# Kernel optimization log

Hardware: AMD Instinct MI355X
Metric: run time of the kernel (lower is better)

Reference implementation:

```python
import jax, jax.numpy as jnp
import numpy as np

EPS = 1e-5

# The 8 fixed sobel kernels from the original module. Summing convolutions with
# the same input equals one convolution with the summed kernel, so we embed the
# four 3x3 kernels (pad=1) into 5x5 (pad=2) and precombine everything into a
# single depthwise 5x5 kernel (exactly the math of detect_edge_1/2 summed).
_K3 = [
    [[2, 4, 2], [0, 0, 0], [-2, -4, -2]],
    [[4, 2, 0], [2, 0, -2], [0, -2, -4]],
    [[2, 0, -2], [4, 0, -4], [2, 0, -2]],
    [[0, -2, -4], [2, 0, -2], [4, 2, 0]],
]
_K5 = [
    [[0, 0, 0, 0, 0], [0, -2, -4, -2, 0], [-1, -4, 0, 4, 1], [0, 2, 4, 2, 0], [0, 0, 0, 0, 0]],
    [[0, 0, -1, 0, 0], [0, -2, -4, 2, 0], [0, -4, 0, 4, 0], [0, -2, 4, 2, 0], [0, 0, 1, 0, 0]],
    [[0, 0, 1, 0, 0], [0, -2, 4, 2, 0], [0, -4, 0, 4, 0], [0, -2, -4, 2, 0], [0, 0, -1, 0, 0]],
    [[0, 0, 0, 0, 0], [0, 2, 4, 2, 0], [-1, -4, 0, 4, 1], [0, -2, -4, -2, 0], [0, 0, 0, 0, 0]],
]

def _combined_sobel_kernel():
    k = np.zeros((5, 5), dtype=np.float32)
    for k3 in _K3:
        k[1:4, 1:4] += np.asarray(k3, dtype=np.float32)
    for k5 in _K5:
        k += np.asarray(k5, dtype=np.float32)
    return jnp.asarray(k)

SOBEL_K = _combined_sobel_kernel()  # [5,5]


def _conv2d(x, w, b, pad):
    # x: [N,C,H,W], w: [O,I,kh,kw]
    y = jax.lax.conv_general_dilated(
        x, w, window_strides=(1, 1), padding=[(pad, pad), (pad, pad)],
        dimension_numbers=('NCHW', 'OIHW', 'NCHW'))
    return y + b[None, :, None, None]


def _bn_relu(y, gamma, beta):
    # BatchNorm2d in training mode: per-channel batch stats over (N,H,W),
    # biased variance, eps=1e-5.
    m = jnp.mean(y, axis=(0, 2, 3), keepdims=True)
    v = jnp.mean(jnp.square(y - m), axis=(0, 2, 3), keepdims=True)
    yn = (y - m) * jax.lax.rsqrt(v + EPS)
    return jax.nn.relu(yn * gamma[None, :, None, None] + beta[None, :, None, None])


def _single_conv(x, w, b, gamma, beta, pad):
    return _bn_relu(_conv2d(x, w, b, pad), gamma, beta)


def _sobel(x):
    # Fused depthwise conv replacing the per-channel loops over 8 kernels.
    C = x.shape[1]
    w = jnp.broadcast_to(SOBEL_K[None, None], (C, 1, 5, 5))
    return jax.lax.conv_general_dilated(
        x, w, window_strides=(1, 1), padding=[(2, 2), (2, 2)],
        dimension_numbers=('NCHW', 'OIHW', 'NCHW'), feature_group_count=C)


def setup_inputs() -> dict:
    key = jax.random.key(0)
    ks = jax.random.split(key, 16)
    Cin, Cout = 64, 128
    Ch = Cout // 2
    B, H, W = 8, 160, 160
    s = 0.05
    d = {
        'input_f': jax.random.normal(ks[0], (B, Cin, H, W), jnp.float32),
        'w1': jax.random.normal(ks[1], (Cout, Cin, 1, 1), jnp.float32) * s,
        'b1': jnp.zeros((Cout,), jnp.float32),
        'g1': jnp.ones((Cout,), jnp.float32),
        'be1': jnp.zeros((Cout,), jnp.float32),
        'w2': jax.random.normal(ks[2], (Ch, Cout, 3, 3), jnp.float32) * s,
        'b2': jnp.zeros((Ch,), jnp.float32),
        'g2': jnp.ones((Ch,), jnp.float32),
        'be2': jnp.zeros((Ch,), jnp.float32),
        'w3': jax.random.normal(ks[3], (Ch, Ch, 3, 3), jnp.float32) * s,
        'b3': jnp.zeros((Ch,), jnp.float32),
        'g3': jnp.ones((Ch,), jnp.float32),
        'be3': jnp.zeros((Ch,), jnp.float32),
        'w4': jax.random.normal(ks[4], (Ch, Cin, 3, 3), jnp.float32) * s,
        'b4': jnp.zeros((Ch,), jnp.float32),
        'g4': jnp.ones((Ch,), jnp.float32),
        'be4': jnp.zeros((Ch,), jnp.float32),
    }
    return d


def reference(input_f, w1, b1, g1, be1, w2, b2, g2, be2, w3, b3, g3, be3, w4, b4, g4, be4):
    c1 = _single_conv(input_f, w1, b1, g1, be1, pad=0)   # [B,Cout,H,W]
    c2 = _single_conv(c1, w2, b2, g2, be2, pad=1)        # [B,Cout//2,H,W]
    edge = _sobel(c2)                                    # depthwise sobel sum
    c3 = _single_conv(edge, w3, b3, g3, be3, pad=1)
    skip = _single_conv(input_f, w4, b4, g4, be4, pad=1)
    return jnp.concatenate([skip, c3], axis=1)           # [B,Cout,H,W]
```

## Files before the change

### kernel.cpp

```cpp
#include <hip/hip_runtime.h>

typedef unsigned short u16;
typedef unsigned int u32;
typedef __attribute__((ext_vector_type(8))) short bf16x8;
typedef __attribute__((ext_vector_type(4))) float f32x4;

#define WD 160
#define HW 25600
#define NPIXF 204800.0f
#define BNEPS 1e-5f
#define SLOTB 6553600ll
#define BATB  13107200ll

__device__ __forceinline__ float bf2f(u16 u){ return __uint_as_float(((u32)u)<<16); }
__device__ __forceinline__ u16 f2bf(float f){ u32 x=__float_as_uint(f); return (u16)((x + 0x7FFFu + ((x>>16)&1u))>>16); }
__device__ __forceinline__ u32 pack2(float a,float b){ return (u32)f2bf(a) | ((u32)f2bf(b)<<16); }

__device__ __forceinline__ f32x4 MF(bf16x8 a, bf16x8 b, f32x4 c){
  return __builtin_amdgcn_mfma_f32_16x16x32_bf16(a, b, c, 0, 0, 0);
}
__device__ __forceinline__ void gload16(const void* g, void* l){
  __builtin_amdgcn_global_load_lds((const __attribute__((address_space(1))) void*)(g),
                                   (__attribute__((address_space(3))) void*)(l), 16, 0, 0);
}

__global__ __launch_bounds__(256) void k_prepw(
    const float* __restrict__ w1, const float* __restrict__ w2,
    const float* __restrict__ w3, const float* __restrict__ w4,
    u16* __restrict__ wp1, u16* __restrict__ wp2,
    u16* __restrict__ wp3, u16* __restrict__ wp4)
{
  int t = blockIdx.x*256 + threadIdx.x;
  if (t < 8192){
    int i = t&7, oc = (t>>3)&127, kc = (t>>10)&3, icb = t>>12;
    wp1[t] = f2bf(w1[oc*64 + icb*32 + kc*8 + i]);
  }
  int u = t - 8192;
  if (u >= 0 && u < 73728){
    int i = u&7, oc = (u>>3)&63, kc = (u>>9)&3, v = u>>11;
    int icb = (v*57)>>9; int tap = v - icb*9;
    wp2[u] = f2bf(w2[(oc*128 + icb*32 + kc*8 + i)*9 + tap]);
  }
  int u3 = t - (8192+73728);
  if (u3 >= 0 && u3 < 36864){
    int k = u3&31, oc = (u3>>5)&63, v = u3>>11;
    int icb = (v >= 9) ? 1 : 0; int tap = v - icb*9;
    wp3[u3] = f2bf(w3[(oc*64 + icb*32 + k)*9 + tap]);
    wp4[u3] = f2bf(w4[(oc*64 + icb*32 + k)*9 + tap]);
  }
}

__global__ __launch_bounds__(256,4) void k_conv1(
    const float* __restrict__ x, const u16* __restrict__ wp1,
    char* __restrict__ dout, float* __restrict__ stats, int nslot)
{
  __shared__ __align__(16) char Xs[16384];
  const int tid = threadIdx.x, lane = tid&63, w = tid>>6;
  const int l15 = lane&15, kc = lane>>4;
  int flat = blockIdx.x + 200*blockIdx.y;
  flat = (flat&7)*200 + (flat>>3);
  const int b = flat/200, bx = flat - b*200;
  const int px0 = bx*128;
  const float* xb = x + (size_t)b*64*HW;

#pragma unroll
  for (int q=0; q<4; ++q){
    int s = q*256 + tid;
    int px = s & 127, ck = (s>>7)&3, icb = s>>9;
    const float* pb = xb + (size_t)(icb*32 + ck*8)*HW + px0 + px;
    u32 w4[4];
#pragma unroll
    for (int j=0;j<4;++j)
      w4[j] = pack2(pb[(size_t)(2*j)*HW], pb[(size_t)(2*j+1)*HW]);
    *(uint4*)(Xs + icb*8192 + px*64 + ((ck ^ ((px>>1)&3))<<4))
        = make_uint4(w4[0],w4[1],w4[2],w4[3]);
  }
  __syncthreads();

  f32x4 acc[4][4];
  for (int t=0;t<4;++t) for (int o=0;o<4;++o) acc[t][o] = (f32x4){0.f,0.f,0.f,0.f};
  const int och = (w>>1)*64;
  int a1off[4];
  for (int t=0;t<4;++t){
    int px = (w&1)*64 + t*16 + l15;
    a1off[t] = px*64 + ((kc ^ ((px>>1)&3))<<4);
  }
  __builtin_amdgcn_s_setprio(1);
#pragma unroll
  for (int icb=0; icb<2; ++icb){
    bf16x8 a[4], bw[4];
#pragma unroll
    for (int t=0;t<4;++t) a[t] = *(const bf16x8*)(Xs + icb*8192 + a1off[t]);
#pragma unroll
    for (int o=0;o<4;++o)
      bw[o] = *(const bf16x8*)(wp1 + ((size_t)(icb*4 + kc)*128 + och + o*16 + l15)*8);
#pragma unroll
    for (int t=0;t<4;++t)
#pragma unroll
      for (int o=0;o<4;++o)
        acc[t][o] = MF(a[t], bw[o], acc[t][o]);
  }
  __builtin_amdgcn_s_setprio(0);

  u16* c1 = (u16*)(dout + (size_t)b*BATB);
  float sa[4]={0,0,0,0}, sq[4]={0,0,0,0};
  for (int t=0;t<4;++t){
    int pxb = px0 + (w&1)*64 + t*16 + kc*4;
    for (int o=0;o<4;++o){
      int oc = och + o*16 + l15;
#pragma unroll
      for (int r=0;r<4;++r){
        float v = acc[t][o][r];
        c1[(size_t)(pxb + r)*128 + oc] = f2bf(v);
        sa[o]+=v; sq[o]+=v*v;
      }
    }
  }
  const int slot = flat & (nslot-1);
  for (int o=0;o<4;++o){
    float s1_=sa[o], s2_=sq[o];
    s1_+=__shfl_xor(s1_,16); s2_+=__shfl_xor(s2_,16);
    s1_+=__shfl_xor(s1_,32); s2_+=__shfl_xor(s2_,32);
    if (lane < 16){
      float* p = stats + ((size_t)slot*128 + och + o*16 + l15)*4;
      atomicAdd(p, s1_); atomicAdd(p+1, s2_);
    }
  }
}

__global__ void k_fold23(const float* __restrict__ s2, const float* __restrict__ s3,
                         float* __restrict__ f23, int nslot){
  int t = threadIdx.x;
  const float* src = (t < 128) ? s2 : s3;
  int c = t & 127;
  float sm=0.f, sq=0.f;
  for (int s=0;s<nslot;++s){ const float* p = src + ((size_t)s*128 + c)*4; sm+=p[0]; sq+=p[1]; }
  f23[t*2] = sm; f23[t*2+1] = sq;
}

__global__ __launch_bounds__(256,4) void k_conv2(
    char* __restrict__ dout, const u16* __restrict__ wp2,
    const float* __restrict__ S0, const float* __restrict__ g1,
    const float* __restrict__ be1,
    float* __restrict__ statsO, int nslot)
{
  __shared__ __align__(16) char Xs[21760];
  __shared__ __align__(16) float scbi[128][2];
  const int tid = threadIdx.x, lane = tid&63, w = tid>>6;
  const int l15 = lane&15, kc = lane>>4;
  int flat = blockIdx.x + 5*(blockIdx.y + 20*blockIdx.z);
  flat = (flat&7)*100 + (flat>>3);
  const int b = flat/100; int r100 = flat - b*100;
  const int by = r100/5, bx = r100 - by*5;
  const int gx0 = bx*32, gy0 = by*8;
  const u16* c1raw = (const u16*)(dout + (size_t)b*BATB);
  u16* raw2 = (u16*)(dout + (size_t)b*BATB + SLOTB);

  if (tid < 128){
    float sm=0.f, sq=0.f;
    for (int s=0;s<nslot;++s){ const float* p = S0 + ((size_t)s*128 + tid)*4; sm+=p[0]; sq+=p[1]; }
    float m = sm/NPIXF;
    float v = sq/NPIXF - m*m;
    float sc = g1[tid]*rsqrtf(v + BNEPS);
    scbi[tid][0] = sc; scbi[tid][1] = be1[tid] - m*sc;
  }

  f32x4 acc[4][4];
  for (int t=0;t<4;++t) for (int o=0;o<4;++o) acc[t][o] = (f32x4){0.f,0.f,0.f,0.f};

  int xon[2][3];
  for (int h=0;h<2;++h) for (int dx=0;dx<3;++dx){
    int xi = l15 + h*16 + dx;
    xon[h][dx] = xi*64 + ((kc ^ ((xi>>1)&3))<<4);
  }

  __syncthreads();
  for (int icb=0; icb<4; ++icb){
    if (icb) __syncthreads();
    for (int s = tid; s < 1360; s += 256){
      int p = s>>2, sub = s&3;
      int yy = (int)(((u32)p*241u)>>13);
      int xi = p - yy*34;
      int gy = gy0 - 1 + yy, gx = gx0 - 1 + xi;
      int c = sub ^ ((xi>>1)&3);
      uint4 o4 = make_uint4(0,0,0,0);
      if ((unsigned)gy < 160u && (unsigned)gx < 160u){
        int cb = icb*32 + c*8;
        uint4 q = *(const uint4*)(c1raw + ((size_t)(gy*WD+gx)*128 + cb));
        u32 ww[4] = {q.x,q.y,q.z,q.w};
        u32 ro[4];
#pragma unroll
        for (int j=0;j<4;++j){
          float lo = bf2f((u16)(ww[j]&0xFFFFu)), hi = bf2f((u16)(ww[j]>>16));
          lo = fmaxf(0.f, lo*scbi[cb+2*j][0]   + scbi[cb+2*j][1]);
          hi = fmaxf(0.f, hi*scbi[cb+2*j+1][0] + scbi[cb+2*j+1][1]);
          ro[j] = pack2(lo, hi);
        }
        o4 = make_uint4(ro[0],ro[1],ro[2],ro[3]);
      }
      *(uint4*)(Xs + p*64 + sub*16) = o4;
    }
    __syncthreads();
    __builtin_amdgcn_s_setprio(1);
#pragma unroll
    for (int tap=0; tap<9; ++tap){
      const int dy = tap/3, dx = tap - dy*3;
      bf16x8 a[4], bw[4];
#pragma unroll
      for (int o=0;o<4;++o)
        bw[o] = *(const bf16x8*)(wp2 + ((size_t)((icb*9 + tap)*4 + kc)*64 + o*16 + l15)*8);
#pragma unroll
      for (int t=0;t<4;++t)
        a[t] = *(const bf16x8*)(Xs + (2*w + (t>>1) + dy)*2176 + xon[t&1][dx]);
#pragma unroll
      for (int t=0;t<4;++t)
#pragma unroll
        for (int o=0;o<4;++o)
          acc[t][o] = MF(a[t], bw[o], acc[t][o]);
    }
    __builtin_amdgcn_s_setprio(0);
  }

  float sa[4]={0,0,0,0}, sq[4]={0,0,0,0};
  for (int t=0;t<4;++t){
    int gy = gy0 + 2*w + (t>>1);
    int gxb = gx0 + (t&1)*16 + kc*4;
    for (int o=0;o<4;++o){
      int oc = o*16 + l15;
#pragma unroll
      for (int r=0;r<4;++r){
        float v = acc[t][o][r];
        raw2[(size_t)(gy*WD + gxb + r)*64 + oc] = f2bf(v);
        sa[o]+=v; sq[o]+=v*v;
      }
    }
  }
  int slot = flat & (nslot-1);
  for (int o=0;o<4;++o){
    float s1_=sa[o], s2_=sq[o];
    s1_+=__shfl_xor(s1_,16); s2_+=__shfl_xor(s2_,16);
    s1_+=__shfl_xor(s1_,32); s2_+=__shfl_xor(s2_,32);
    if (lane<16){
      float* p = statsO + ((size_t)slot*128 + o*16 + l15)*4;
      atomicAdd(p,s1_); atomicAdd(p+1,s2_);
    }
  }
}

__global__ __launch_bounds__(256) void k_sobel(
    char* __restrict__ dout, const float* __restrict__ S1,
    const float* __restrict__ g2, const float* __restrict__ be2,
    u16* __restrict__ edge_base, long ebstride, int nslot)
{
  __shared__ float ascS[8], abiS[8];
  int tid = threadIdx.x;
  int flat = blockIdx.x + 100*(blockIdx.y + 8*blockIdx.z);
  flat = (flat&7)*800 + (flat>>3);
  int b = flat/800; int r800 = flat - b*800;
  int cb = r800/100, bxx = r800 - cb*100;
  if (tid < 64){
    int c = cb*8 + (tid&7);
    float sm=0.f, sq=0.f;
    for (int s = tid>>3; s < nslot; s += 8){
      const float* p = S1 + ((size_t)s*128 + c)*4;
      sm += p[0]; sq += p[1];
    }
    sm += __shfl_xor(sm, 8);  sq += __shfl_xor(sq, 8);
    sm += __shfl_xor(sm, 16); sq += __shfl_xor(sq, 16);
    sm += __shfl_xor(sm, 32); sq += __shfl_xor(sq, 32);
    if (tid < 8){
      float m = sm/NPIXF, v = sq/NPIXF - m*m;
      float sc = g2[c]*rsqrtf(v+BNEPS);
      ascS[tid] = sc; abiS[tid] = be2[c] - m*sc;
    }
  }
  __syncthreads();
  int px = bxx*256 + tid;
  int y = (int)(((u32)px*52429u)>>23);
  int x = px - y*WD;
  const u16* raw2 = (const u16*)(dout + (size_t)b*BATB + SLOTB);
  u16* edge = edge_base + (size_t)b*ebstride;
  float av[8] = {0,0,0,0,0,0,0,0};
  auto TAP = [&](int dy, int dx, float wt){
    int yy = y+dy, xx = x+dx;
    if ((unsigned)yy>=160u || (unsigned)xx>=160u) return;
    uint4 q = *(const uint4*)(raw2 + ((size_t)(yy*WD+xx)*64 + cb*8));
    u32 ww[4] = {q.x,q.y,q.z,q.w};
#pragma unroll
    for (int j=0;j<4;++j){
      float lo = bf2f((u16)(ww[j]&0xFFFFu)), hi = bf2f((u16)(ww[j]>>16));
      lo = fmaxf(0.f, lo*ascS[2*j]   + abiS[2*j]);
      hi = fmaxf(0.f, hi*ascS[2*j+1] + abiS[2*j+1]);
      av[2*j]   += wt*lo;
      av[2*j+1] += wt*hi;
    }
  };
  TAP(-1,-1,4.f); TAP(-1,0,4.f);
  TAP(0,-2,-2.f); TAP(0,-1,-8.f); TAP(0,1,8.f); TAP(0,2,2.f);
  TAP(1,0,-4.f);  TAP(1,1,-4.f);
  uint4 o;
  o.x = pack2(av[0],av[1]); o.y = pack2(av[2],av[3]);
  o.z = pack2(av[4],av[5]); o.w = pack2(av[6],av[7]);
  *(uint4*)(edge + ((size_t)px*64 + cb*8)) = o;
}

__global__ __launch_bounds__(256,3) void k_conv34(
    char* __restrict__ dout, const float* __restrict__ x,
    const u16* __restrict__ wp3, const u16* __restrict__ wp4,
    float* __restrict__ st3, float* __restrict__ st4,
    const u16* __restrict__ zeros, const u16* __restrict__ edge_base,
    long ebstride, int nslot, int mode)
{
  __shared__ __align__(16) char Xs[49152];
  const int tid = threadIdx.x, lane = tid&63, w = tid>>6;
  const int l15 = lane&15, kc = lane>>4;
  int bx, by, bzz, flat;
  if (mode == 2){
    flat = blockIdx.x + 5*(blockIdx.y + 20*blockIdx.z);
    flat = (flat&7)*200 + (flat>>3);
    bzz = flat/100; int r100 = flat - bzz*100; by = r100/5; bx = r100 - by*5;
  } else { bx = blockIdx.x; by = blockIdx.y; bzz = blockIdx.z;
           flat = bx + 5*(by + 20*bzz); }
  int b, job;
  if (mode == 2){ b = bzz>>1; job = bzz&1; } else { b = bzz; job = mode; }
  const int gx0 = bx*32, gy0 = by*8;
  const u16* wp = job ? wp4 : wp3;
  float* statsO = job ? st4 : st3;
  float* out = job ? (float*)(dout + (size_t)b*BATB)
                   : (float*)(dout + (size_t)b*BATB + SLOTB);
  const float* xb = x + (size_t)b*64*HW;
  const u16* edge = edge_base + (size_t)b*ebstride;

  if (job){
    for (int s = tid; s < 2720; s += 256){
      int icb = (s >= 1360) ? 1 : 0;
      int sl = s - icb*1360;
      int ck = (sl>=680) ? ((sl>=1020)?3:2) : ((sl>=340)?1:0);
      int pp = sl - ck*340;
      int yq = (int)(((u32)pp*241u)>>13);
      int xi = pp - yq*34;
      int gy = gy0-1+yq, gx = gx0-1+xi;
      u32 w4[4] = {0,0,0,0};
      if ((unsigned)gy<160u && (unsigned)gx<160u){
        const float* pb = xb + (size_t)(icb*32 + ck*8)*HW + gy*WD + gx;
#pragma unroll
        for (int j=0;j<4;++j)
          w4[j] = pack2(pb[(size_t)(2*j)*HW], pb[(size_t)(2*j+1)*HW]);
      }
      *(uint4*)(Xs + icb*24576 + pp*64 + ((ck ^ ((xi>>1)&3))<<4))
          = make_uint4(w4[0],w4[1],w4[2],w4[3]);
    }
    __syncthreads();
  } else {
#pragma unroll
    for (int icb=0; icb<2; ++icb)
#pragma unroll
      for (int it=0; it<6; ++it){
        int s = it*256 + tid;
        int p = s>>2, sub = s&3;
        int yy = (int)(((u32)p*241u)>>13);
        int xi = p - yy*34;
        int gy = gy0-1+yy, gx = gx0-1+xi;
        int c = sub ^ ((xi>>1)&3);
        const u16* src = zeros + ((tid&63)<<3);
        if (p<340 && (unsigned)gy<160u && (unsigned)gx<160u)
          src = edge + ((size_t)(gy*WD+gx)*64 + icb*32 + c*8);
        gload16(src, Xs + icb*24576 + (it*256 + (tid & ~63))*16);
      }
    asm volatile("s_waitcnt vmcnt(6)\n\ts_barrier" ::: "memory");
  }

  f32x4 acc[4][4];
  for (int m=0;m<4;++m) for (int t=0;t<4;++t) acc[m][t] = (f32x4){0.f,0.f,0.f,0.f};
  int xon[2][3];
  for (int h=0;h<2;++h) for (int dx=0;dx<3;++dx){
    int xi = l15 + h*16 + dx;
    xon[h][dx] = xi*64 + ((kc ^ ((xi>>1)&3))<<4);
  }

  for (int icb=0; icb<2; ++icb){
    if (icb == 1 && job == 0)
      asm volatile("s_waitcnt vmcnt(0)\n\ts_barrier" ::: "memory");
    __builtin_amdgcn_s_setprio(1);
#pragma unroll
    for (int tap=0; tap<9; ++tap){
      const int dy = tap/3, dx = tap - dy*3;
      bf16x8 a[4], bv[4];
#pragma unroll
      for (int m=0;m<4;++m)
        a[m] = *(const bf16x8*)(wp + ((size_t)((icb*9+tap)*64 + m*16 + l15)*32 + kc*8));
#pragma unroll
      for (int t=0;t<4;++t)
        bv[t] = *(const bf16x8*)(Xs + icb*24576 + (2*w + (t>>1) + dy)*2176 + xon[t&1][dx]);
#pragma unroll
      for (int m=0;m<4;++m)
#pragma unroll
        for (int t=0;t<4;++t)
          acc[m][t] = MF(a[m], bv[t], acc[m][t]);
    }
    __builtin_amdgcn_s_setprio(0);
  }

  float sa[4][4], sq[4][4];
  for (int m=0;m<4;++m) for (int r=0;r<4;++r){ sa[m][r]=0.f; sq[m][r]=0.f; }
  for (int m=0;m<4;++m){
    for (int t=0;t<4;++t){
      int gy = gy0 + 2*w + (t>>1);
      int gx = gx0 + (t&1)*16 + l15;
#pragma unroll
      for (int r=0;r<4;++r){
        float v = acc[m][t][r];
        out[(size_t)(m*16 + kc*4 + r)*HW + gy*WD + gx] = v;
        sa[m][r]+=v; sq[m][r]+=v*v;
      }
    }
  }
  int slot = flat & (nslot-1);
  for (int m=0;m<4;++m)
    for (int r=0;r<4;++r){
      float s1_=sa[m][r], s2_=sq[m][r];
      s1_+=__shfl_xor(s1_,1); s2_+=__shfl_xor(s2_,1);
      s1_+=__shfl_xor(s1_,2); s2_+=__shfl_xor(s2_,2);
      s1_+=__shfl_xor(s1_,4); s2_+=__shfl_xor(s2_,4);
      s1_+=__shfl_xor(s1_,8); s2_+=__shfl_xor(s2_,8);
      if (l15==0){
        float* p = statsO + ((size_t)slot*128 + m*16 + kc*4 + r)*4;
        atomicAdd(p,s1_); atomicAdd(p+1,s2_);
      }
    }
}

__global__ __launch_bounds__(256) void k_bnrelu(
    float* __restrict__ io, const float* __restrict__ f23,
    const float* __restrict__ g3, const float* __restrict__ be3,
    const float* __restrict__ g4, const float* __restrict__ be4)
{
  size_t e = ((size_t)blockIdx.x*256 + threadIdx.x)*8;
  int cg = (int)((e/HW) & 127);
  float* p = io + (size_t)blockIdx.y*3276800 + e;
  float sm,sq,gg,bb;
  if (cg>=64){ int c=cg-64; sm=f23[c*2]; sq=f23[c*2+1]; gg=g3[c]; bb=be3[c]; }
  else       { sm=f23[(128+cg)*2]; sq=f23[(128+cg)*2+1]; gg=g4[cg]; bb=be4[cg]; }
  float m = sm/NPIXF;
  float v = sq/NPIXF - m*m;
  float sc = gg*rsqrtf(v + BNEPS);
  float bi = bb - m*sc;
  float4 a = *(float4*)p;
  float4 bq = *(float4*)(p+4);
  a.x=fmaxf(0.f,a.x*sc+bi); a.y=fmaxf(0.f,a.y*sc+bi);
  a.z=fmaxf(0.f,a.z*sc+bi); a.w=fmaxf(0.f,a.w*sc+bi);
  bq.x=fmaxf(0.f,bq.x*sc+bi); bq.y=fmaxf(0.f,bq.y*sc+bi);
  bq.z=fmaxf(0.f,bq.z*sc+bi); bq.w=fmaxf(0.f,bq.w*sc+bi);
  *(float4*)p = a;
  *(float4*)(p+4) = bq;
}

extern "C" void kernel_launch(void* const* d_in, const int* in_sizes, int n_in,
                              void* d_out, int out_size, void* d_ws, size_t ws_size,
                              hipStream_t stream)
{
  const float* x   = (const float*)d_in[0];
  const float* w1  = (const float*)d_in[1];
  const float* g1  = (const float*)d_in[3];
  const float* be1 = (const float*)d_in[4];
  const float* w2  = (const float*)d_in[5];
  const float* g2  = (const float*)d_in[7];
  const float* be2 = (const float*)d_in[8];
  const float* w3  = (const float*)d_in[9];
  const float* g3  = (const float*)d_in[11];
  const float* be3 = (const float*)d_in[12];
  const float* w4  = (const float*)d_in[13];
  const float* g4  = (const float*)d_in[15];
  const float* be4 = (const float*)d_in[16];
  (void)in_sizes; (void)n_in; (void)out_size;

  int nslot = 32;
  auto need = [&](int ns)->size_t{
    return (size_t)4*ns*128*4*4 + 4096 + (size_t)(8192+73728+36864+36864)*2 + 1024;
  };
  while (nslot > 1 && need(nslot) > ws_size) nslot >>= 1;
  if (need(nslot) > ws_size) return;

  char* ws = (char*)d_ws;
  float* S = (float*)ws;
  size_t stg = (size_t)nslot*128*4;
  float* S0=S, *S1=S+stg, *S2=S+2*stg, *S3=S+3*stg;
  float* F = S + 4*stg;
  u16* wp1 = (u16*)(F + 1024);
  u16* wp2 = wp1 + 8192;
  u16* wp3 = wp2 + 73728;
  u16* wp4 = wp3 + 36864;
  u16* zeros = wp4 + 36864;
  size_t base = need(nslot);
  bool big = (ws_size >= base + 26214400ull);
  u16* edge_base;
  long ebstride;
  if (big){ edge_base = (u16*)(ws + base); ebstride = 64L*HW; }
  else    { edge_base = (u16*)((char*)d_out + 3276800); ebstride = BATB/2; }

  hipMemsetAsync(S, 0, 4*stg*sizeof(float), stream);
  hipMemsetAsync(zeros, 0, 1024, stream);

  k_prepw<<<464, 256, 0, stream>>>(w1, w2, w3, w4, wp1, wp2, wp3, wp4);
  k_conv1<<<dim3(200,8), 256, 0, stream>>>(x, wp1, (char*)d_out, S0, nslot);
  k_conv2<<<dim3(5,20,8), 256, 0, stream>>>((char*)d_out, wp2, S0, g1, be1, S1, nslot);
  k_sobel<<<dim3(100,8,8), 256, 0, stream>>>((char*)d_out, S1, g2, be2, edge_base, ebstride, nslot);
  if (big){
    k_conv34<<<dim3(5,20,16), 256, 0, stream>>>((char*)d_out, x, wp3, wp4, S2, S3,
                                                zeros, edge_base, ebstride, nslot, 2);
  } else {
    k_conv34<<<dim3(5,20,8), 256, 0, stream>>>((char*)d_out, x, wp3, wp4, S2, S3,
                                               zeros, edge_base, ebstride, nslot, 0);
    k_conv34<<<dim3(5,20,8), 256, 0, stream>>>((char*)d_out, x, wp3, wp4, S2, S3,
                                               zeros, edge_base, ebstride, nslot, 1);
  }
  k_fold23<<<1, 256, 0, stream>>>(S2, S3, F, nslot);
  k_bnrelu<<<dim3(1600,8), 256, 0, stream>>>((float*)d_out, F, g3, be3, g4, be4);
}
```

Measured before the change: 359.0 us.

## Pre-transpose input to bf16 NHWC and single-buffer conv34 LDS

Adds a transpose kernel that converts the fp32 NCHW input into a bf16 pixel-major buffer in workspace when space allows. conv1 then reads MFMA operands straight from global memory, and the skip conv (conv4) stages its tiles with async LDS loads like the edge path, replacing strided fp32 gathers. conv34 now stages one 32-channel block at a time, which halves its LDS use and raises occupancy to 4, and the setprio hints are dropped. In exchange it adds an extra kernel launch and 52MB more workspace traffic, and the two channel blocks no longer overlap their loads.

```diff
diff --git a/kernel.cpp b/kernel.cpp
--- a/kernel.cpp
+++ b/kernel.cpp
@@ -50,7 +50,89 @@
   }
 }
 
-__global__ __launch_bounds__(256,4) void k_conv1(
+__global__ __launch_bounds__(256,2) void k_xpose(
+    const float* __restrict__ x, u16* __restrict__ xb16)
+{
+  __shared__ u32 T[256][33];
+  const int tid = threadIdx.x, b = blockIdx.y, px0 = blockIdx.x*256;
+  const float* xb = x + (size_t)b*64*HW;
+#pragma unroll 8
+  for (int c2=0; c2<32; ++c2){
+    float v0 = xb[(size_t)(2*c2)*HW + px0 + tid];
+    float v1 = xb[(size_t)(2*c2+1)*HW + px0 + tid];
+    T[tid][c2] = pack2(v0, v1);
+  }
+  __syncthreads();
+  u16* ob = xb16 + ((size_t)b*HW + px0)*64;
+#pragma unroll
+  for (int it=0; it<8; ++it){
+    int s = it*256 + tid;
+    int px = s>>3, j = s&7;
+    uint4 q;
+    q.x = T[px][j*4]; q.y = T[px][j*4+1]; q.z = T[px][j*4+2]; q.w = T[px][j*4+3];
+    *(uint4*)(ob + (size_t)px*64 + j*8) = q;
+  }
+}
+
+__global__ __launch_bounds__(256,4) void k_conv1A(
+    const u16* __restrict__ xb16, const u16* __restrict__ wp1,
+    char* __restrict__ dout, float* __restrict__ stats, int nslot)
+{
+  const int tid = threadIdx.x, lane = tid&63, w = tid>>6;
+  const int l15 = lane&15, kc = lane>>4;
+  int flat = blockIdx.x + 200*blockIdx.y;
+  flat = (flat&7)*200 + (flat>>3);
+  const int b = flat/200, bx = flat - b*200;
+  const int px0 = bx*128;
+
+  f32x4 acc[4][4];
+  for (int t=0;t<4;++t) for (int o=0;o<4;++o) acc[t][o] = (f32x4){0.f,0.f,0.f,0.f};
+  const int och = (w>>1)*64;
+  const u16* xrow = xb16 + ((size_t)b*HW + px0 + (w&1)*64)*64;
+
+#pragma unroll
+  for (int icb=0; icb<2; ++icb){
+    bf16x8 a[4], bw[4];
+#pragma unroll
+    for (int t=0;t<4;++t)
+      a[t] = *(const bf16x8*)(xrow + (size_t)(t*16 + l15)*64 + icb*32 + kc*8);
+#pragma unroll
+    for (int o=0;o<4;++o)
+      bw[o] = *(const bf16x8*)(wp1 + ((size_t)(icb*4 + kc)*128 + och + o*16 + l15)*8);
+#pragma unroll
+    for (int t=0;t<4;++t)
+#pragma unroll
+      for (int o=0;o<4;++o)
+        acc[t][o] = MF(a[t], bw[o], acc[t][o]);
+  }
+
+  u16* c1 = (u16*)(dout + (size_t)b*BATB);
+  float sa[4]={0,0,0,0}, sq[4]={0,0,0,0};
+  for (int t=0;t<4;++t){
+    int pxb = px0 + (w&1)*64 + t*16 + kc*4;
+    for (int o=0;o<4;++o){
+      int oc = och + o*16 + l15;
+#pragma unroll
+      for (int r=0;r<4;++r){
+        float v = acc[t][o][r];
+        c1[(size_t)(pxb + r)*128 + oc] = f2bf(v);
+        sa[o]+=v; sq[o]+=v*v;
+      }
+    }
+  }
+  const int slot = flat & (nslot-1);
+  for (int o=0;o<4;++o){
+    float s1_=sa[o], s2_=sq[o];
+    s1_+=__shfl_xor(s1_,16); s2_+=__shfl_xor(s2_,16);
+    s1_+=__shfl_xor(s1_,32); s2_+=__shfl_xor(s2_,32);
+    if (lane < 16){
+      float* p = stats + ((size_t)slot*128 + och + o*16 + l15)*4;
+      atomicAdd(p, s1_); atomicAdd(p+1, s2_);
+    }
+  }
+}
+
+__global__ __launch_bounds__(256,4) void k_conv1B(
     const float* __restrict__ x, const u16* __restrict__ wp1,
     char* __restrict__ dout, float* __restrict__ stats, int nslot)
 {
@@ -85,7 +167,6 @@
     int px = (w&1)*64 + t*16 + l15;
     a1off[t] = px*64 + ((kc ^ ((px>>1)&3))<<4);
   }
-  __builtin_amdgcn_s_setprio(1);
 #pragma unroll
   for (int icb=0; icb<2; ++icb){
     bf16x8 a[4], bw[4];
@@ -100,7 +181,6 @@
       for (int o=0;o<4;++o)
         acc[t][o] = MF(a[t], bw[o], acc[t][o]);
   }
-  __builtin_amdgcn_s_setprio(0);
 
   u16* c1 = (u16*)(dout + (size_t)b*BATB);
   float sa[4]={0,0,0,0}, sq[4]={0,0,0,0};
@@ -304,14 +384,15 @@
   *(uint4*)(edge + ((size_t)px*64 + cb*8)) = o;
 }
 
-__global__ __launch_bounds__(256,3) void k_conv34(
+__global__ __launch_bounds__(256,4) void k_conv34(
     char* __restrict__ dout, const float* __restrict__ x,
+    const u16* __restrict__ xb16,
     const u16* __restrict__ wp3, const u16* __restrict__ wp4,
     float* __restrict__ st3, float* __restrict__ st4,
     const u16* __restrict__ zeros, const u16* __restrict__ edge_base,
     long ebstride, int nslot, int mode)
 {
-  __shared__ __align__(16) char Xs[49152];
+  __shared__ __align__(16) char Xs[24576];
   const int tid = threadIdx.x, lane = tid&63, w = tid>>6;
   const int l15 = lane&15, kc = lane>>4;
   int bx, by, bzz, flat;
@@ -330,30 +411,37 @@
                    : (float*)(dout + (size_t)b*BATB + SLOTB);
   const float* xb = x + (size_t)b*64*HW;
   const u16* edge = edge_base + (size_t)b*ebstride;
-
-  if (job){
-    for (int s = tid; s < 2720; s += 256){
-      int icb = (s >= 1360) ? 1 : 0;
-      int sl = s - icb*1360;
-      int ck = (sl>=680) ? ((sl>=1020)?3:2) : ((sl>=340)?1:0);
-      int pp = sl - ck*340;
-      int yq = (int)(((u32)pp*241u)>>13);
-      int xi = pp - yq*34;
-      int gy = gy0-1+yq, gx = gx0-1+xi;
-      u32 w4[4] = {0,0,0,0};
-      if ((unsigned)gy<160u && (unsigned)gx<160u){
-        const float* pb = xb + (size_t)(icb*32 + ck*8)*HW + gy*WD + gx;
-#pragma unroll
-        for (int j=0;j<4;++j)
-          w4[j] = pack2(pb[(size_t)(2*j)*HW], pb[(size_t)(2*j+1)*HW]);
-      }
-      *(uint4*)(Xs + icb*24576 + pp*64 + ((ck ^ ((xi>>1)&3))<<4))
-          = make_uint4(w4[0],w4[1],w4[2],w4[3]);
-    }
-    __syncthreads();
-  } else {
-#pragma unroll
-    for (int icb=0; icb<2; ++icb)
+  const u16* xsrc = job ? (xb16 ? xb16 + (size_t)b*HW*64 : nullptr) : edge;
+
+  f32x4 acc[4][4];
+  for (int m=0;m<4;++m) for (int t=0;t<4;++t) acc[m][t] = (f32x4){0.f,0.f,0.f,0.f};
+  int xon[2][3];
+  for (int h=0;h<2;++h) for (int dx=0;dx<3;++dx){
+    int xi = l15 + h*16 + dx;
+    xon[h][dx] = xi*64 + ((kc ^ ((xi>>1)&3))<<4);
+  }
+
+  for (int icb=0; icb<2; ++icb){
+    if (icb) __syncthreads();
+    if (job == 1 && !xb16){
+      for (int s = tid; s < 1360; s += 256){
+        int ck = (s>=680) ? ((s>=1020)?3:2) : ((s>=340)?1:0);
+        int pp = s - ck*340;
+        int yq = (int)(((u32)pp*241u)>>13);
+        int xi = pp - yq*34;
+        int gy = gy0-1+yq, gx = gx0-1+xi;
+        u32 w4[4] = {0,0,0,0};
+        if ((unsigned)gy<160u && (unsigned)gx<160u){
+          const float* pb = xb + (size_t)(icb*32 + ck*8)*HW + gy*WD + gx;
+#pragma unroll
+          for (int j=0;j<4;++j)
+            w4[j] = pack2(pb[(size_t)(2*j)*HW], pb[(size_t)(2*j+1)*HW]);
+        }
+        *(uint4*)(Xs + pp*64 + ((ck ^ ((xi>>1)&3))<<4))
+            = make_uint4(w4[0],w4[1],w4[2],w4[3]);
+      }
+      __syncthreads();
+    } else {
 #pragma unroll
       for (int it=0; it<6; ++it){
         int s = it*256 + tid;
@@ -364,24 +452,13 @@
         int c = sub ^ ((xi>>1)&3);
         const u16* src = zeros + ((tid&63)<<3);
         if (p<340 && (unsigned)gy<160u && (unsigned)gx<160u)
-          src = edge + ((size_t)(gy*WD+gx)*64 + icb*32 + c*8);
-        gload16(src, Xs + icb*24576 + (it*256 + (tid & ~63))*16);
-      }
-    asm volatile("s_waitcnt vmcnt(6)\n\ts_barrier" ::: "memory");
-  }
-
-  f32x4 acc[4][4];
-  for (int m=0;m<4;++m) for (int t=0;t<4;++t) acc[m][t] = (f32x4){0.f,0.f,0.f,0.f};
-  int xon[2][3];
-  for (int h=0;h<2;++h) for (int dx=0;dx<3;++dx){
-    int xi = l15 + h*16 + dx;
-    xon[h][dx] = xi*64 + ((kc ^ ((xi>>1)&3))<<4);
-  }
-
-  for (int icb=0; icb<2; ++icb){
-    if (icb == 1 && job == 0)
-      asm volatile("s_waitcnt vmcnt(0)\n\ts_barrier" ::: "memory");
-    __builtin_amdgcn_s_setprio(1);
+          src = xsrc + ((size_t)(gy*WD+gx)*64 + icb*32 + c*8);
+        gload16(src, Xs + (it*256 + (tid & ~63))*16);
+      }
+      asm volatile("s_waitcnt vmcnt(0)" ::: "memory");
+      __syncthreads();
+    }
+
 #pragma unroll
     for (int tap=0; tap<9; ++tap){
       const int dy = tap/3, dx = tap - dy*3;
@@ -391,14 +468,13 @@
         a[m] = *(const bf16x8*)(wp + ((size_t)((icb*9+tap)*64 + m*16 + l15)*32 + kc*8));
 #pragma unroll
       for (int t=0;t<4;++t)
-        bv[t] = *(const bf16x8*)(Xs + icb*24576 + (2*w + (t>>1) + dy)*2176 + xon[t&1][dx]);
+        bv[t] = *(const bf16x8*)(Xs + (2*w + (t>>1) + dy)*2176 + xon[t&1][dx]);
 #pragma unroll
       for (int m=0;m<4;++m)
 #pragma unroll
         for (int t=0;t<4;++t)
           acc[m][t] = MF(a[m], bv[t], acc[m][t]);
     }
-    __builtin_amdgcn_s_setprio(0);
   }
 
   float sa[4][4], sq[4][4];
@@ -492,26 +568,33 @@
   u16* wp4 = wp3 + 36864;
   u16* zeros = wp4 + 36864;
   size_t base = need(nslot);
-  bool big = (ws_size >= base + 26214400ull);
+  bool bigB = (ws_size >= base + 26214400ull);
+  bool bigA = (ws_size >= base + 52428800ull);
   u16* edge_base;
   long ebstride;
-  if (big){ edge_base = (u16*)(ws + base); ebstride = 64L*HW; }
-  else    { edge_base = (u16*)((char*)d_out + 3276800); ebstride = BATB/2; }
+  if (bigB){ edge_base = (u16*)(ws + base); ebstride = 64L*HW; }
+  else     { edge_base = (u16*)((char*)d_out + 3276800); ebstride = BATB/2; }
+  u16* xb16 = bigA ? (u16*)(ws + base + 26214400) : nullptr;
 
   hipMemsetAsync(S, 0, 4*stg*sizeof(float), stream);
   hipMemsetAsync(zeros, 0, 1024, stream);
 
   k_prepw<<<464, 256, 0, stream>>>(w1, w2, w3, w4, wp1, wp2, wp3, wp4);
-  k_conv1<<<dim3(200,8), 256, 0, stream>>>(x, wp1, (char*)d_out, S0, nslot);
+  if (bigA){
+    k_xpose<<<dim3(100,8), 256, 0, stream>>>(x, xb16);
+    k_conv1A<<<dim3(200,8), 256, 0, stream>>>(xb16, wp1, (char*)d_out, S0, nslot);
+  } else {
+    k_conv1B<<<dim3(200,8), 256, 0, stream>>>(x, wp1, (char*)d_out, S0, nslot);
+  }
   k_conv2<<<dim3(5,20,8), 256, 0, stream>>>((char*)d_out, wp2, S0, g1, be1, S1, nslot);
   k_sobel<<<dim3(100,8,8), 256, 0, stream>>>((char*)d_out, S1, g2, be2, edge_base, ebstride, nslot);
-  if (big){
-    k_conv34<<<dim3(5,20,16), 256, 0, stream>>>((char*)d_out, x, wp3, wp4, S2, S3,
+  if (bigB){
+    k_conv34<<<dim3(5,20,16), 256, 0, stream>>>((char*)d_out, x, xb16, wp3, wp4, S2, S3,
                                                 zeros, edge_base, ebstride, nslot, 2);
   } else {
-    k_conv34<<<dim3(5,20,8), 256, 0, stream>>>((char*)d_out, x, wp3, wp4, S2, S3,
+    k_conv34<<<dim3(5,20,8), 256, 0, stream>>>((char*)d_out, x, nullptr, wp3, wp4, S2, S3,
                                                zeros, edge_base, ebstride, nslot, 0);
-    k_conv34<<<dim3(5,20,8), 256, 0, stream>>>((char*)d_out, x, wp3, wp4, S2, S3,
+    k_conv34<<<dim3(5,20,8), 256, 0, stream>>>((char*)d_out, x, nullptr, wp3, wp4, S2, S3,
                                                zeros, edge_base, ebstride, nslot, 1);
   }
   k_fold23<<<1, 256, 0, stream>>>(S2, S3, F, nslot);
```

After: 378.8 us. +5.5%, slower.

## Fuse sobel and BN2-ReLU into conv3 tile load, drop separate sobel kernel

Applied to the files above, without the earlier changes.

When the workspace is large enough, conv2 writes its raw output into the workspace, and the conv3 job computes BN2+ReLU and the 8-tap combined sobel stencil directly while staging its input tile into LDS. This removes the separate k_sobel pass and its edge buffer round-trip. It also rewrites the conv4 input staging into finer two-channel loads, removes the setprio hints, and simplifies block-index swizzles. The cost is redundant stencil reads of neighbouring pixels per tile, extra ALU in the load phase, and occupancy lowered to 2 blocks per CU.

```diff
diff --git a/kernel.cpp b/kernel.cpp
--- a/kernel.cpp
+++ b/kernel.cpp
@@ -85,7 +85,6 @@
     int px = (w&1)*64 + t*16 + l15;
     a1off[t] = px*64 + ((kc ^ ((px>>1)&3))<<4);
   }
-  __builtin_amdgcn_s_setprio(1);
 #pragma unroll
   for (int icb=0; icb<2; ++icb){
     bf16x8 a[4], bw[4];
@@ -100,7 +99,6 @@
       for (int o=0;o<4;++o)
         acc[t][o] = MF(a[t], bw[o], acc[t][o]);
   }
-  __builtin_amdgcn_s_setprio(0);
 
   u16* c1 = (u16*)(dout + (size_t)b*BATB);
   float sa[4]={0,0,0,0}, sq[4]={0,0,0,0};
@@ -142,6 +140,7 @@
     char* __restrict__ dout, const u16* __restrict__ wp2,
     const float* __restrict__ S0, const float* __restrict__ g1,
     const float* __restrict__ be1,
+    u16* __restrict__ raw2base, long r2stride,
     float* __restrict__ statsO, int nslot)
 {
   __shared__ __align__(16) char Xs[21760];
@@ -154,7 +153,7 @@
   const int by = r100/5, bx = r100 - by*5;
   const int gx0 = bx*32, gy0 = by*8;
   const u16* c1raw = (const u16*)(dout + (size_t)b*BATB);
-  u16* raw2 = (u16*)(dout + (size_t)b*BATB + SLOTB);
+  u16* raw2 = raw2base + (size_t)b*r2stride;
 
   if (tid < 128){
     float sm=0.f, sq=0.f;
@@ -201,7 +200,6 @@
       *(uint4*)(Xs + p*64 + sub*16) = o4;
     }
     __syncthreads();
-    __builtin_amdgcn_s_setprio(1);
 #pragma unroll
     for (int tap=0; tap<9; ++tap){
       const int dy = tap/3, dx = tap - dy*3;
@@ -218,7 +216,6 @@
         for (int o=0;o<4;++o)
           acc[t][o] = MF(a[t], bw[o], acc[t][o]);
     }
-    __builtin_amdgcn_s_setprio(0);
   }
 
   float sa[4]={0,0,0,0}, sq[4]={0,0,0,0};
@@ -254,10 +251,7 @@
 {
   __shared__ float ascS[8], abiS[8];
   int tid = threadIdx.x;
-  int flat = blockIdx.x + 100*(blockIdx.y + 8*blockIdx.z);
-  flat = (flat&7)*800 + (flat>>3);
-  int b = flat/800; int r800 = flat - b*800;
-  int cb = r800/100, bxx = r800 - cb*100;
+  int b = blockIdx.z, cb = blockIdx.y;
   if (tid < 64){
     int c = cb*8 + (tid&7);
     float sm=0.f, sq=0.f;
@@ -275,7 +269,7 @@
     }
   }
   __syncthreads();
-  int px = bxx*256 + tid;
+  int px = blockIdx.x*256 + tid;
   int y = (int)(((u32)px*52429u)>>23);
   int x = px - y*WD;
   const u16* raw2 = (const u16*)(dout + (size_t)b*BATB + SLOTB);
@@ -304,70 +298,117 @@
   *(uint4*)(edge + ((size_t)px*64 + cb*8)) = o;
 }
 
-__global__ __launch_bounds__(256,3) void k_conv34(
+__global__ __launch_bounds__(256,2) void k_conv34(
     char* __restrict__ dout, const float* __restrict__ x,
+    const u16* __restrict__ raw2b, long r2stride,
+    const float* __restrict__ S1, const float* __restrict__ g2,
+    const float* __restrict__ be2,
     const u16* __restrict__ wp3, const u16* __restrict__ wp4,
     float* __restrict__ st3, float* __restrict__ st4,
     const u16* __restrict__ zeros, const u16* __restrict__ edge_base,
     long ebstride, int nslot, int mode)
 {
   __shared__ __align__(16) char Xs[49152];
+  __shared__ float scbi2[64][2];
   const int tid = threadIdx.x, lane = tid&63, w = tid>>6;
   const int l15 = lane&15, kc = lane>>4;
-  int bx, by, bzz, flat;
-  if (mode == 2){
-    flat = blockIdx.x + 5*(blockIdx.y + 20*blockIdx.z);
-    flat = (flat&7)*200 + (flat>>3);
-    bzz = flat/100; int r100 = flat - bzz*100; by = r100/5; bx = r100 - by*5;
-  } else { bx = blockIdx.x; by = blockIdx.y; bzz = blockIdx.z;
-           flat = bx + 5*(by + 20*bzz); }
   int b, job;
-  if (mode == 2){ b = bzz>>1; job = bzz&1; } else { b = bzz; job = mode; }
-  const int gx0 = bx*32, gy0 = by*8;
+  if (mode == 2){ b = blockIdx.z>>1; job = blockIdx.z&1; }
+  else          { b = blockIdx.z;    job = mode; }
+  const int gx0 = blockIdx.x*32, gy0 = blockIdx.y*8;
+  const int flat = blockIdx.x + 5*(blockIdx.y + 20*blockIdx.z);
   const u16* wp = job ? wp4 : wp3;
   float* statsO = job ? st4 : st3;
   float* out = job ? (float*)(dout + (size_t)b*BATB)
                    : (float*)(dout + (size_t)b*BATB + SLOTB);
-  const float* xb = x + (size_t)b*64*HW;
-  const u16* edge = edge_base + (size_t)b*ebstride;
+
+  if (job == 0 && raw2b){
+    if (tid < 64){
+      float sm=0.f, sq=0.f;
+      for (int s=0;s<nslot;++s){ const float* p = S1 + ((size_t)s*128 + tid)*4; sm+=p[0]; sq+=p[1]; }
+      float m = sm/NPIXF, v = sq/NPIXF - m*m;
+      float sc = g2[tid]*rsqrtf(v + BNEPS);
+      scbi2[tid][0] = sc; scbi2[tid][1] = be2[tid] - m*sc;
+    }
+    __syncthreads();
+  }
 
   if (job){
+    const float* xb = x + (size_t)b*64*HW;
+#pragma unroll 4
+    for (int it=0; it<43; ++it){
+      int s = it*256 + tid; if (s >= 10880) break;
+      int icb = (s >= 5440) ? 1 : 0;
+      int sl = s - icb*5440;
+      int yq = (int)(((u32)(sl>>5)*965u)>>14);
+      int rem = sl - yq*544;
+      int icp = (int)(((u32)rem*241u)>>13);
+      int xi = rem - icp*34;
+      int gy = gy0-1+yq, gx = gx0-1+xi;
+      float v0=0.f, v1=0.f;
+      if ((unsigned)gy<160u && (unsigned)gx<160u){
+        const float* p = xb + (size_t)(icb*32 + icp*2)*HW + gy*WD + gx;
+        v0 = p[0]; v1 = p[HW];
+      }
+      int phys = icb*24576 + (yq*34 + xi)*64 + (((icp>>2) ^ ((xi>>1)&3))<<4) + (icp&3)*4;
+      *(u32*)(Xs + phys) = pack2(v0, v1);
+    }
+    __syncthreads();
+  } else if (raw2b){
+    const u16* r2 = raw2b + (size_t)b*r2stride;
     for (int s = tid; s < 2720; s += 256){
       int icb = (s >= 1360) ? 1 : 0;
       int sl = s - icb*1360;
-      int ck = (sl>=680) ? ((sl>=1020)?3:2) : ((sl>=340)?1:0);
-      int pp = sl - ck*340;
-      int yq = (int)(((u32)pp*241u)>>13);
-      int xi = pp - yq*34;
-      int gy = gy0-1+yq, gx = gx0-1+xi;
-      u32 w4[4] = {0,0,0,0};
+      int p = sl>>2, sub = sl&3;
+      int yy = (int)(((u32)p*241u)>>13);
+      int xi = p - yy*34;
+      int gy = gy0-1+yy, gx = gx0-1+xi;
+      int c = sub ^ ((xi>>1)&3);
+      int cb = icb*32 + c*8;
+      float av[8] = {0,0,0,0,0,0,0,0};
       if ((unsigned)gy<160u && (unsigned)gx<160u){
-        const float* pb = xb + (size_t)(icb*32 + ck*8)*HW + gy*WD + gx;
-#pragma unroll
-        for (int j=0;j<4;++j)
-          w4[j] = pack2(pb[(size_t)(2*j)*HW], pb[(size_t)(2*j+1)*HW]);
-      }
-      *(uint4*)(Xs + icb*24576 + pp*64 + ((ck ^ ((xi>>1)&3))<<4))
-          = make_uint4(w4[0],w4[1],w4[2],w4[3]);
+        auto TAP = [&](int dy, int dxv, float wt){
+          int yy2 = gy+dy, xx2 = gx+dxv;
+          if ((unsigned)yy2>=160u || (unsigned)xx2>=160u) return;
+          uint4 q = *(const uint4*)(r2 + ((size_t)(yy2*WD+xx2))*64 + cb);
+          u32 ww[4] = {q.x,q.y,q.z,q.w};
+#pragma unroll
+          for (int j=0;j<4;++j){
+            float lo = bf2f((u16)(ww[j]&0xFFFFu)), hi = bf2f((u16)(ww[j]>>16));
+            lo = fmaxf(0.f, lo*scbi2[cb+2*j][0]   + scbi2[cb+2*j][1]);
+            hi = fmaxf(0.f, hi*scbi2[cb+2*j+1][0] + scbi2[cb+2*j+1][1]);
+            av[2*j]   += wt*lo;
+            av[2*j+1] += wt*hi;
+          }
+        };
+        TAP(-1,-1,4.f); TAP(-1,0,4.f);
+        TAP(0,-2,-2.f); TAP(0,-1,-8.f); TAP(0,1,8.f); TAP(0,2,2.f);
+        TAP(1,0,-4.f);  TAP(1,1,-4.f);
+      }
+      uint4 o;
+      o.x = pack2(av[0],av[1]); o.y = pack2(av[2],av[3]);
+      o.z = pack2(av[4],av[5]); o.w = pack2(av[6],av[7]);
+      *(uint4*)(Xs + icb*24576 + p*64 + sub*16) = o;
     }
     __syncthreads();
   } else {
-#pragma unroll
-    for (int icb=0; icb<2; ++icb)
-#pragma unroll
-      for (int it=0; it<6; ++it){
-        int s = it*256 + tid;
-        int p = s>>2, sub = s&3;
-        int yy = (int)(((u32)p*241u)>>13);
-        int xi = p - yy*34;
-        int gy = gy0-1+yy, gx = gx0-1+xi;
-        int c = sub ^ ((xi>>1)&3);
-        const u16* src = zeros + ((tid&63)<<3);
-        if (p<340 && (unsigned)gy<160u && (unsigned)gx<160u)
-          src = edge + ((size_t)(gy*WD+gx)*64 + icb*32 + c*8);
-        gload16(src, Xs + icb*24576 + (it*256 + (tid & ~63))*16);
-      }
-    asm volatile("s_waitcnt vmcnt(6)\n\ts_barrier" ::: "memory");
+    const u16* edge = edge_base + (size_t)b*ebstride;
+    for (int it=0; it<12; ++it){
+      int s = it*256 + tid;
+      int icb = (s >= 1536) ? 1 : 0;
+      int sl = s - icb*1536;
+      int p = sl>>2, sub = sl&3;
+      int yy = (int)(((u32)p*241u)>>13);
+      int xi = p - yy*34;
+      int gy = gy0-1+yy, gx = gx0-1+xi;
+      int c = sub ^ ((xi>>1)&3);
+      const u16* src = zeros + ((tid&63)<<3);
+      if (p<340 && (unsigned)gy<160u && (unsigned)gx<160u)
+        src = edge + ((size_t)(gy*WD+gx)*64 + icb*32 + c*8);
+      gload16(src, Xs + (it*256 + (tid & ~63))*16);
+    }
+    asm volatile("s_waitcnt vmcnt(0)" ::: "memory");
+    __syncthreads();
   }
 
   f32x4 acc[4][4];
@@ -378,10 +419,8 @@
     xon[h][dx] = xi*64 + ((kc ^ ((xi>>1)&3))<<4);
   }
 
+#pragma unroll
   for (int icb=0; icb<2; ++icb){
-    if (icb == 1 && job == 0)
-      asm volatile("s_waitcnt vmcnt(0)\n\ts_barrier" ::: "memory");
-    __builtin_amdgcn_s_setprio(1);
 #pragma unroll
     for (int tap=0; tap<9; ++tap){
       const int dy = tap/3, dx = tap - dy*3;
@@ -398,7 +437,6 @@
         for (int t=0;t<4;++t)
           acc[m][t] = MF(a[m], bv[t], acc[m][t]);
     }
-    __builtin_amdgcn_s_setprio(0);
   }
 
   float sa[4][4], sq[4][4];
@@ -492,26 +530,33 @@
   u16* wp4 = wp3 + 36864;
   u16* zeros = wp4 + 36864;
   size_t base = need(nslot);
-  bool big = (ws_size >= base + 26214400ull);
-  u16* edge_base;
-  long ebstride;
-  if (big){ edge_base = (u16*)(ws + base); ebstride = 64L*HW; }
-  else    { edge_base = (u16*)((char*)d_out + 3276800); ebstride = BATB/2; }
+  bool bigWS = (ws_size >= base + 26214400ull);
+
+  u16* raw2base; long r2stride;
+  if (bigWS){ raw2base = (u16*)(ws + base); r2stride = 64L*HW; }
+  else      { raw2base = (u16*)((char*)d_out + SLOTB); r2stride = BATB/2; }
+  u16* edge_base = (u16*)((char*)d_out + 3276800);
+  long ebstride = BATB/2;
 
   hipMemsetAsync(S, 0, 4*stg*sizeof(float), stream);
   hipMemsetAsync(zeros, 0, 1024, stream);
 
   k_prepw<<<464, 256, 0, stream>>>(w1, w2, w3, w4, wp1, wp2, wp3, wp4);
   k_conv1<<<dim3(200,8), 256, 0, stream>>>(x, wp1, (char*)d_out, S0, nslot);
-  k_conv2<<<dim3(5,20,8), 256, 0, stream>>>((char*)d_out, wp2, S0, g1, be1, S1, nslot);
-  k_sobel<<<dim3(100,8,8), 256, 0, stream>>>((char*)d_out, S1, g2, be2, edge_base, ebstride, nslot);
-  if (big){
-    k_conv34<<<dim3(5,20,16), 256, 0, stream>>>((char*)d_out, x, wp3, wp4, S2, S3,
-                                                zeros, edge_base, ebstride, nslot, 2);
+  k_conv2<<<dim3(5,20,8), 256, 0, stream>>>((char*)d_out, wp2, S0, g1, be1,
+                                            raw2base, r2stride, S1, nslot);
+  if (bigWS){
+    k_conv34<<<dim3(5,20,16), 256, 0, stream>>>((char*)d_out, x, raw2base, r2stride,
+                                                S1, g2, be2, wp3, wp4, S2, S3,
+                                                zeros, nullptr, 0, nslot, 2);
   } else {
-    k_conv34<<<dim3(5,20,8), 256, 0, stream>>>((char*)d_out, x, wp3, wp4, S2, S3,
+    k_sobel<<<dim3(100,8,8), 256, 0, stream>>>((char*)d_out, S1, g2, be2,
+                                               edge_base, ebstride, nslot);
+    k_conv34<<<dim3(5,20,8), 256, 0, stream>>>((char*)d_out, x, nullptr, 0,
+                                               S1, g2, be2, wp3, wp4, S2, S3,
                                                zeros, edge_base, ebstride, nslot, 0);
-    k_conv34<<<dim3(5,20,8), 256, 0, stream>>>((char*)d_out, x, wp3, wp4, S2, S3,
+    k_conv34<<<dim3(5,20,8), 256, 0, stream>>>((char*)d_out, x, nullptr, 0,
+                                               S1, g2, be2, wp3, wp4, S2, S3,
                                                zeros, edge_base, ebstride, nslot, 1);
   }
   k_fold23<<<1, 256, 0, stream>>>(S2, S3, F, nslot);
```

Result: faster. 335.2 us (-6.6%).
